# Performance work log

Hardware: AMD Instinct MI355X
Metric: run time of the kernel (lower is better)

Reference implementation:

```python
import jax, jax.numpy as jnp
import numpy as np

CUTOFF = 5.0
NUM_RADIAL = 6
HIDDEN = 128
N_NODES = 100000
N_EDGES = 800000
MAX_Z = 95
P = 6  # envelope_exponent(5) + 1, per PyG Envelope


def _envelope(x):
    # PyG DimeNet Envelope: (1/x + a*x^(p-1) + b*x^p + c*x^(p+1)) * (x < 1)
    a = -(P + 1) * (P + 2) / 2.0   # -28
    b = P * (P + 2)                # 48
    c = -P * (P + 1) / 2.0         # -21
    xp0 = x ** (P - 1)
    xp1 = xp0 * x
    xp2 = xp1 * x
    return (1.0 / x + a * xp0 + b * xp1 + c * xp2) * (x < 1.0)


def setup_inputs():
    key = jax.random.key(0)
    ks = jax.random.split(key, 8)
    z = jax.random.randint(ks[0], (N_NODES,), 0, MAX_Z, dtype=jnp.int32)
    pos = jax.random.normal(ks[1], (N_NODES, 3), dtype=jnp.float32)
    ei = jax.random.randint(ks[2], (2, N_EDGES), 0, N_NODES, dtype=jnp.int32)
    i, j = ei[0], ei[1]
    j = jnp.where(j == i, (j + 1) % N_NODES, j)  # radius_graph emits no self-loops (avoids d=0)
    edge_index = jnp.stack([i, j])
    # BesselBasisLayer learnable frequencies: pi * n
    freq = np.pi * jnp.arange(1, NUM_RADIAL + 1, dtype=jnp.float32)
    s3 = float(np.sqrt(3.0))
    emb_table = jax.random.uniform(ks[3], (MAX_Z, HIDDEN), jnp.float32, -s3, s3)
    W_rbf = jax.random.normal(ks[4], (NUM_RADIAL, HIDDEN), jnp.float32) * (1.0 / np.sqrt(NUM_RADIAL))
    b_rbf = jnp.zeros((HIDDEN,), jnp.float32)
    W_lin = jax.random.normal(ks[5], (3 * HIDDEN, HIDDEN), jnp.float32) * (1.0 / np.sqrt(3 * HIDDEN))
    b_lin = jnp.zeros((HIDDEN,), jnp.float32)
    return {"z": z, "pos": pos, "edge_index": edge_index, "freq": freq,
            "emb_table": emb_table, "W_rbf": W_rbf, "b_rbf": b_rbf,
            "W_lin": W_lin, "b_lin": b_lin}


def reference(z, pos, edge_index, freq, emb_table, W_rbf, b_rbf, W_lin, b_lin):
    n = z.shape[0]
    i, j = edge_index[0], edge_index[1]
    # per-edge distance  [E]
    d = jnp.sqrt(jnp.sum((pos[i] - pos[j]) ** 2, axis=-1))
    # Bessel RBF  [E, num_radial]
    x = d[:, None] / CUTOFF
    rbf = _envelope(x) * jnp.sin(freq * x)
    # DimeNet EmbeddingBlock (act = SiLU/swish)
    h_rbf = jax.nn.silu(rbf @ W_rbf + b_rbf)            # [E, H]
    xz = emb_table[z]                                    # [N, H]
    e_emb = jax.nn.silu(
        jnp.concatenate([xz[i], xz[j], h_rbf], axis=-1) @ W_lin + b_lin
    )                                                    # [E, H]
    # scatter_mean over target node j -> [N, H]
    sums = jax.ops.segment_sum(e_emb, j, num_segments=n)
    cnt = jax.ops.segment_sum(jnp.ones_like(d), j, num_segments=n)
    v_emb = sums / jnp.maximum(cnt, 1.0)[:, None]
    return v_emb  # pool=None -> node-level embeddings
```

## Files before the change

kernel.cpp:

```cpp
#include <hip/hip_runtime.h>
#include <hip/hip_bf16.h>
#include <math.h>

#define HID 128
#define NRAD 6
#define TABN 4096
#define CUTOFF_INV 0.2f
#define MZ 95
#define MZP (MZ + 1)
#define SENT ((MZ << 13) | (MZ << 20))
#define PAD 32
#define OVF_CAP 65536
#define FTR 8
#define LOG2E 1.4426950408889634f
#define LN2   0.6931471805599453f

typedef unsigned int uint32;
typedef __attribute__((ext_vector_type(2))) float f2;

__global__ void build1(const float* __restrict__ emb, const float* __restrict__ W_lin,
                       const float* __restrict__ freq, const float* __restrict__ W_rbf,
                       const float* __restrict__ b_rbf, const float* __restrict__ b_lin,
                       const int* __restrict__ ei, const float* __restrict__ pos,
                       const int* __restrict__ z,
                       __hip_bfloat16* __restrict__ Tb, float* __restrict__ ftab,
                       int* __restrict__ cnt, int* __restrict__ payload,
                       int* __restrict__ ovfcnt, int2* __restrict__ ovfbuf,
                       int MAXZ, int E) {
    __shared__ float sh[FTR * HID];
    int h   = threadIdx.x;
    int bid = blockIdx.x;
    int nT  = 2 * (MAXZ + 1);
    int nF  = (TABN + FTR) / FTR;
    if (bid < nT) {
        int zz = bid >> 1, s = bid & 1;
        if (zz == MAXZ) {
            Tb[(size_t)(s * (MAXZ + 1) + zz) * HID + h] = __float2bfloat16(-86.5f);
            return;
        }
        sh[h] = emb[zz * HID + h];
        __syncthreads();
        const float* W = W_lin + (size_t)s * HID * HID;
        float acc = (s == 0) ? b_lin[h] : 0.f;
#pragma unroll 8
        for (int k = 0; k < HID; ++k) acc = fmaf(sh[k], W[k * HID + h], acc);
        Tb[(size_t)(s * (MAXZ + 1) + zz) * HID + h] = __float2bfloat16(acc * LOG2E);
    } else if (bid < nT + nF) {
        int t0 = (bid - nT) * FTR;
        for (int r = 0; r < FTR; ++r) {
            int t = t0 + r;
            float rbf[NRAD];
            if (t == 0) {
#pragma unroll
                for (int k = 0; k < NRAD; ++k) rbf[k] = freq[k];
            } else if (t >= TABN) {
#pragma unroll
                for (int k = 0; k < NRAD; ++k) rbf[k] = 0.f;
            } else {
                float x  = (float)t / (float)TABN;
                float x2 = x * x, x5 = x2 * x2 * x;
                float env = 1.f / x + x5 * (-28.f + x * (48.f + x * (-21.f)));
#pragma unroll
                for (int k = 0; k < NRAD; ++k) rbf[k] = env * sinf(freq[k] * x);
            }
            float pre = b_rbf[h];
#pragma unroll
            for (int k = 0; k < NRAD; ++k) pre = fmaf(rbf[k], W_rbf[k * HID + h], pre);
            sh[r * HID + h] = pre / (1.f + __expf(-pre));
        }
        __syncthreads();
        const float* W3 = W_lin + (size_t)2 * HID * HID;
        float acc[FTR];
#pragma unroll
        for (int r = 0; r < FTR; ++r) acc[r] = 0.f;
#pragma unroll 4
        for (int k = 0; k < HID; ++k) {
            float w = W3[k * HID + h];
#pragma unroll
            for (int r = 0; r < FTR; ++r) acc[r] = fmaf(sh[r * HID + k], w, acc[r]);
        }
        for (int r = 0; r < FTR; ++r) {
            int t = t0 + r;
            if (t <= TABN) ftab[(size_t)t * HID + h] = acc[r] * LOG2E;
        }
    } else {
        int e = (bid - nT - nF) * HID + h;
        if (e < E) {
            int i = ei[e];
            int j = ei[E + e];
            float dx = pos[3 * i]     - pos[3 * j];
            float dy = pos[3 * i + 1] - pos[3 * j + 1];
            float dz = pos[3 * i + 2] - pos[3 * j + 2];
            float d  = sqrtf(dx * dx + dy * dy + dz * dz);
            float u  = fminf(d * CUTOFF_INV, 1.0f) * (float)TABN;
            int   ti = (int)(u + 0.5f);
            if (ti > TABN) ti = TABN;
            int pl = ti | (z[i] << 13) | (z[j] << 20);
            int r  = atomicAdd(&cnt[j], 1);
            if (r < PAD) {
                payload[(size_t)j * PAD + r] = pl;
            } else {
                int o = atomicAdd(ovfcnt, 1);
                if (o < OVF_CAP) ovfbuf[o] = make_int2(j, pl);
            }
        }
    }
}

__device__ __forceinline__ float exp2neg(float x) {
    float r; asm("v_exp_f32 %0, -%1" : "=v"(r) : "v"(x)); return r;
}

#define RL(pv_, idx_) __builtin_amdgcn_readlane((pv_), (idx_))

#define FLOAD(pl_) (*(const f2*)((const char*)ftab + (uint32)((((pl_) & 0x1FFF) << 9) + fbyte)))

#define TLA(pl_) sT[((((pl_) >> 13) & 0x7F) << 6) + lane]
#define TLB(pl_) sT[sB + ((((pl_) >> 20) & 0x7F) << 6) + lane]

#define COMPUTE(f_, ua_, ub_) do {                                             \
    f2 A_, B_, P_, E_, R_;                                                     \
    A_.x = __uint_as_float((ua_) << 16);                                       \
    A_.y = __uint_as_float((ua_) & 0xFFFF0000u);                               \
    B_.x = __uint_as_float((ub_) << 16);                                       \
    B_.y = __uint_as_float((ub_) & 0xFFFF0000u);                               \
    P_ = (A_ + B_) + f_;                                  \
    E_.x = exp2neg(P_.x);  E_.y = exp2neg(P_.y);                               \
    E_ = E_ + onev;                                              \
    R_.x = __builtin_amdgcn_rcpf(E_.x);                                        \
    R_.y = __builtin_amdgcn_rcpf(E_.y);                                        \
    acc = __builtin_elementwise_fma(P_, R_, acc);            \
} while (0)

__launch_bounds__(1024)
__global__ void gather_k(const int* __restrict__ cnt, const int* __restrict__ payload,
                         const uint32* __restrict__ Tb32, const float* __restrict__ ftab,
                         const int* __restrict__ ovfcnt, const int2* __restrict__ ovfbuf,
                         float* __restrict__ out, int N) {
    __shared__ uint32 sT[2 * MZP * (HID / 2)];
    int tid = threadIdx.x;
    for (int k = tid; k < 2 * MZP * (HID / 2); k += 1024) sT[k] = Tb32[k];
    __syncthreads();

    const int sB = MZP * (HID / 2);
    int lane = tid & 63;
    int l32  = lane & 31;
    int wv   = __builtin_amdgcn_readfirstlane(tid >> 6);
    uint32 fbyte = (uint32)lane << 3;
    f2 onev; onev.x = 1.f; onev.y = 1.f;
    int nov  = __builtin_amdgcn_readfirstlane(*ovfcnt);
    if (nov > OVF_CAP) nov = OVF_CAP;
    int nW = gridDim.x << 4;

    int n = (blockIdx.x << 4) + wv;
    int degC = 0, plvC = SENT;
    if (n < N) {
        degC = __builtin_amdgcn_readfirstlane(cnt[n]);
        plvC = payload[(size_t)n * PAD + l32];
    }

    while (n < N) {
        int n2 = n + nW;
        int degN = 0, plvN = SENT;
        if (n2 < N) {
            degN = __builtin_amdgcn_readfirstlane(cnt[n2]);
            plvN = payload[(size_t)n2 * PAD + l32];
        }

        int deg = degC;
        int cb  = deg < PAD ? deg : PAD;
        int plv = (l32 < cb) ? plvC : SENT;

        f2 acc; acc.x = 0.f; acc.y = 0.f;
        if (cb > 0) {
            int pl0 = RL(plv, 0), pl1 = RL(plv, 1), pl2 = RL(plv, 2);
            f2 g0 = FLOAD(pl0), g1 = FLOAD(pl1), g2 = FLOAD(pl2);
            uint32 ua0 = TLA(pl0), ub0 = TLB(pl0);
            uint32 ua1 = TLA(pl1), ub1 = TLB(pl1);
#pragma unroll 4
            for (int k = 0; k < cb; ++k) {
                int pl3 = RL(plv, k + 3);
                f2 g3 = FLOAD(pl3);
                uint32 ua2 = TLA(pl2), ub2 = TLB(pl2);
                COMPUTE(g0, ua0, ub0);
                g0 = g1; g1 = g2; g2 = g3;
                ua0 = ua1; ub0 = ub1;
                ua1 = ua2; ub1 = ub2;
                pl2 = pl3;
            }
        }
        if (deg > PAD && nov > 0) {
            for (int o = 0; o < nov; ++o) {
                int2 v = ovfbuf[o];
                int jn = __builtin_amdgcn_readfirstlane(v.x);
                if (jn == n) {
                    int pl = __builtin_amdgcn_readfirstlane(v.y);
                    f2 f_ = FLOAD(pl);
                    uint32 ua_ = TLA(pl), ub_ = TLB(pl);
                    COMPUTE(f_, ua_, ub_);
                }
            }
        }
        float s = (deg > 0) ? LN2 / (float)deg : 0.0f;
        f2 o2; o2.x = acc.x * s; o2.y = acc.y * s;
        *(f2*)(out + (size_t)n * HID + (lane << 1)) = o2;
        n = n2; degC = degN; plvC = plvN;
    }
}

extern "C" void kernel_launch(void* const* d_in, const int* in_sizes, int n_in,
                              void* d_out, int out_size, void* d_ws, size_t ws_size,
                              hipStream_t stream) {
    const int*   z     = (const int*)d_in[0];
    const float* pos   = (const float*)d_in[1];
    const int*   ei    = (const int*)d_in[2];
    const float* freq  = (const float*)d_in[3];
    const float* emb   = (const float*)d_in[4];
    const float* W_rbf = (const float*)d_in[5];
    const float* b_rbf = (const float*)d_in[6];
    const float* W_lin = (const float*)d_in[7];
    const float* b_lin = (const float*)d_in[8];

    int N    = in_sizes[0];
    int E    = in_sizes[2] / 2;
    int MAXZ = in_sizes[4] / HID;
    float* out = (float*)d_out;

    int N_pad = ((N + 1024) / 1024) * 1024;

    char* ws = (char*)d_ws;
    size_t off = 0;
    auto alloc = [&](size_t bytes) { char* p = ws + off; off = (off + bytes + 255) & ~(size_t)255; return p; };
    int*   cnt     = (int*)alloc((size_t)N_pad * 4);
    int*   ovfcnt  = (int*)alloc(256);
    __hip_bfloat16* Tb = (__hip_bfloat16*)alloc((size_t)2 * (MAXZ + 1) * HID * 2);
    float* ftab    = (float*)alloc((size_t)(TABN + 1) * HID * 4);
    int*   payload = (int*)alloc((size_t)N_pad * PAD * 4);
    int2*  ovfbuf  = (int2*)alloc((size_t)OVF_CAP * 8);

    hipMemsetAsync(cnt, 0, (size_t)N_pad * 4 + 256, stream);

    int nBuild = 2 * (MAXZ + 1) + (TABN + FTR) / FTR + (E + HID - 1) / HID;
    build1<<<nBuild, HID, 0, stream>>>(emb, W_lin, freq, W_rbf, b_rbf, b_lin,
                                       ei, pos, z, Tb, ftab, cnt, payload,
                                       ovfcnt, ovfbuf, MAXZ, E);
    gather_k<<<512, 1024, 0, stream>>>(cnt, payload, (const uint32*)Tb, ftab,
                                       ovfcnt, ovfbuf, out, N);
}
```

Baseline: 178.6 us.

## Pack pos and z into float4, hoist target-node table term out of gather loop

```diff
diff --git a/kernel.cpp b/kernel.cpp
--- a/kernel.cpp
+++ b/kernel.cpp
@@ -8,7 +8,7 @@
 #define CUTOFF_INV 0.2f
 #define MZ 95
 #define MZP (MZ + 1)
-#define SENT ((MZ << 13) | (MZ << 20))
+#define SENTI (MZ << 13)
 #define PAD 32
 #define OVF_CAP 65536
 #define FTR 8
@@ -18,11 +18,26 @@
 typedef unsigned int uint32;
 typedef __attribute__((ext_vector_type(2))) float f2;
 
+__global__ void zpack_k(const float* __restrict__ pos, const int* __restrict__ z,
+                        float4* __restrict__ pos4, int* __restrict__ cnt,
+                        int* __restrict__ ovfcnt, int N) {
+    int n = blockIdx.x * 256 + threadIdx.x;
+    if (blockIdx.x == 0 && threadIdx.x == 0) *ovfcnt = 0;
+    if (n < N) {
+        float4 p;
+        p.x = pos[3 * n];
+        p.y = pos[3 * n + 1];
+        p.z = pos[3 * n + 2];
+        p.w = __int_as_float(z[n]);
+        pos4[n] = p;
+        cnt[n]  = 0;
+    }
+}
+
 __global__ void build1(const float* __restrict__ emb, const float* __restrict__ W_lin,
                        const float* __restrict__ freq, const float* __restrict__ W_rbf,
                        const float* __restrict__ b_rbf, const float* __restrict__ b_lin,
-                       const int* __restrict__ ei, const float* __restrict__ pos,
-                       const int* __restrict__ z,
+                       const int* __restrict__ ei, const float4* __restrict__ pos4,
                        __hip_bfloat16* __restrict__ Tb, float* __restrict__ ftab,
                        int* __restrict__ cnt, int* __restrict__ payload,
                        int* __restrict__ ovfcnt, int2* __restrict__ ovfbuf,
@@ -84,24 +99,36 @@
             if (t <= TABN) ftab[(size_t)t * HID + h] = acc[r] * LOG2E;
         }
     } else {
-        int e = (bid - nT - nF) * HID + h;
-        if (e < E) {
-            int i = ei[e];
-            int j = ei[E + e];
-            float dx = pos[3 * i]     - pos[3 * j];
-            float dy = pos[3 * i + 1] - pos[3 * j + 1];
-            float dz = pos[3 * i + 2] - pos[3 * j + 2];
-            float d  = sqrtf(dx * dx + dy * dy + dz * dz);
-            float u  = fminf(d * CUTOFF_INV, 1.0f) * (float)TABN;
-            int   ti = (int)(u + 0.5f);
-            if (ti > TABN) ti = TABN;
-            int pl = ti | (z[i] << 13) | (z[j] << 20);
-            int r  = atomicAdd(&cnt[j], 1);
-            if (r < PAD) {
-                payload[(size_t)j * PAD + r] = pl;
-            } else {
-                int o = atomicAdd(ovfcnt, 1);
-                if (o < OVF_CAP) ovfbuf[o] = make_int2(j, pl);
+        int t  = (bid - nT - nF) * HID + h;
+        int Eh = (E + 1) >> 1;
+        if (t < Eh) {
+            int  e1   = t + Eh;
+            bool has1 = e1 < E;
+            int i0 = ei[t],  j0 = ei[E + t];
+            int i1 = has1 ? ei[e1] : i0, j1 = has1 ? ei[E + e1] : j0;
+            float4 a0 = pos4[i0], b0 = pos4[j0];
+            float4 a1 = pos4[i1], b1 = pos4[j1];
+
+            float dx0 = a0.x - b0.x, dy0 = a0.y - b0.y, dz0 = a0.z - b0.z;
+            float d0  = sqrtf(dx0 * dx0 + dy0 * dy0 + dz0 * dz0);
+            float u0  = fminf(d0 * CUTOFF_INV, 1.0f) * (float)TABN;
+            int   ti0 = (int)(u0 + 0.5f);
+            if (ti0 > TABN) ti0 = TABN;
+            int pl0 = ti0 | (__float_as_int(a0.w) << 13);
+            int r0  = atomicAdd(&cnt[j0], 1);
+            if (r0 < PAD) payload[(size_t)j0 * PAD + r0] = pl0;
+            else { int o = atomicAdd(ovfcnt, 1); if (o < OVF_CAP) ovfbuf[o] = make_int2(j0, pl0); }
+
+            if (has1) {
+                float dx1 = a1.x - b1.x, dy1 = a1.y - b1.y, dz1 = a1.z - b1.z;
+                float d1  = sqrtf(dx1 * dx1 + dy1 * dy1 + dz1 * dz1);
+                float u1  = fminf(d1 * CUTOFF_INV, 1.0f) * (float)TABN;
+                int   ti1 = (int)(u1 + 0.5f);
+                if (ti1 > TABN) ti1 = TABN;
+                int pl1 = ti1 | (__float_as_int(a1.w) << 13);
+                int r1  = atomicAdd(&cnt[j1], 1);
+                if (r1 < PAD) payload[(size_t)j1 * PAD + r1] = pl1;
+                else { int o = atomicAdd(ovfcnt, 1); if (o < OVF_CAP) ovfbuf[o] = make_int2(j1, pl1); }
             }
         }
     }
@@ -116,15 +143,12 @@
 #define FLOAD(pl_) (*(const f2*)((const char*)ftab + (uint32)((((pl_) & 0x1FFF) << 9) + fbyte)))
 
 #define TLA(pl_) sT[((((pl_) >> 13) & 0x7F) << 6) + lane]
-#define TLB(pl_) sT[sB + ((((pl_) >> 20) & 0x7F) << 6) + lane]
-
-#define COMPUTE(f_, ua_, ub_) do {                                             \
-    f2 A_, B_, P_, E_, R_;                                                     \
+
+#define COMPUTE(f_, ua_) do {                                                  \
+    f2 A_, P_, E_, R_;                                                         \
     A_.x = __uint_as_float((ua_) << 16);                                       \
     A_.y = __uint_as_float((ua_) & 0xFFFF0000u);                               \
-    B_.x = __uint_as_float((ub_) << 16);                                       \
-    B_.y = __uint_as_float((ub_) & 0xFFFF0000u);                               \
-    P_ = (A_ + B_) + f_;                                  \
+    P_ = (A_ + Bv) + f_;                                  \
     E_.x = exp2neg(P_.x);  E_.y = exp2neg(P_.y);                               \
     E_ = E_ + onev;                                              \
     R_.x = __builtin_amdgcn_rcpf(E_.x);                                        \
@@ -135,14 +159,15 @@
 __launch_bounds__(1024)
 __global__ void gather_k(const int* __restrict__ cnt, const int* __restrict__ payload,
                          const uint32* __restrict__ Tb32, const float* __restrict__ ftab,
+                         const int* __restrict__ z,
                          const int* __restrict__ ovfcnt, const int2* __restrict__ ovfbuf,
                          float* __restrict__ out, int N) {
-    __shared__ uint32 sT[2 * MZP * (HID / 2)];
+    __shared__ uint32 sT[MZP * (HID / 2)];
     int tid = threadIdx.x;
-    for (int k = tid; k < 2 * MZP * (HID / 2); k += 1024) sT[k] = Tb32[k];
+    for (int k = tid; k < MZP * (HID / 2); k += 1024) sT[k] = Tb32[k];
     __syncthreads();
 
-    const int sB = MZP * (HID / 2);
+    const uint32* T2g = Tb32 + MZP * (HID / 2);
     int lane = tid & 63;
     int l32  = lane & 31;
     int wv   = __builtin_amdgcn_readfirstlane(tid >> 6);
@@ -153,39 +178,45 @@
     int nW = gridDim.x << 4;
 
     int n = (blockIdx.x << 4) + wv;
-    int degC = 0, plvC = SENT;
+    int degC = 0, plvC = SENTI; uint32 ubC = 0;
     if (n < N) {
         degC = __builtin_amdgcn_readfirstlane(cnt[n]);
         plvC = payload[(size_t)n * PAD + l32];
+        int zn = __builtin_amdgcn_readfirstlane(z[n]);
+        ubC  = T2g[(zn << 6) + lane];
     }
 
     while (n < N) {
         int n2 = n + nW;
-        int degN = 0, plvN = SENT;
+        int degN = 0, plvN = SENTI; uint32 ubN = 0;
         if (n2 < N) {
             degN = __builtin_amdgcn_readfirstlane(cnt[n2]);
             plvN = payload[(size_t)n2 * PAD + l32];
+            int zn2 = __builtin_amdgcn_readfirstlane(z[n2]);
+            ubN  = T2g[(zn2 << 6) + lane];
         }
 
         int deg = degC;
         int cb  = deg < PAD ? deg : PAD;
-        int plv = (l32 < cb) ? plvC : SENT;
+        int plv = (l32 < cb) ? plvC : SENTI;
+        f2 Bv;
+        Bv.x = __uint_as_float(ubC << 16);
+        Bv.y = __uint_as_float(ubC & 0xFFFF0000u);
 
         f2 acc; acc.x = 0.f; acc.y = 0.f;
         if (cb > 0) {
             int pl0 = RL(plv, 0), pl1 = RL(plv, 1), pl2 = RL(plv, 2);
             f2 g0 = FLOAD(pl0), g1 = FLOAD(pl1), g2 = FLOAD(pl2);
-            uint32 ua0 = TLA(pl0), ub0 = TLB(pl0);
-            uint32 ua1 = TLA(pl1), ub1 = TLB(pl1);
+            uint32 ua0 = TLA(pl0);
+            uint32 ua1 = TLA(pl1);
 #pragma unroll 4
             for (int k = 0; k < cb; ++k) {
                 int pl3 = RL(plv, k + 3);
                 f2 g3 = FLOAD(pl3);
-                uint32 ua2 = TLA(pl2), ub2 = TLB(pl2);
-                COMPUTE(g0, ua0, ub0);
+                uint32 ua2 = TLA(pl2);
+                COMPUTE(g0, ua0);
                 g0 = g1; g1 = g2; g2 = g3;
-                ua0 = ua1; ub0 = ub1;
-                ua1 = ua2; ub1 = ub2;
+                ua0 = ua1; ua1 = ua2;
                 pl2 = pl3;
             }
         }
@@ -196,15 +227,15 @@
                 if (jn == n) {
                     int pl = __builtin_amdgcn_readfirstlane(v.y);
                     f2 f_ = FLOAD(pl);
-                    uint32 ua_ = TLA(pl), ub_ = TLB(pl);
-                    COMPUTE(f_, ua_, ub_);
+                    uint32 ua_ = TLA(pl);
+                    COMPUTE(f_, ua_);
                 }
             }
         }
         float s = (deg > 0) ? LN2 / (float)deg : 0.0f;
         f2 o2; o2.x = acc.x * s; o2.y = acc.y * s;
         *(f2*)(out + (size_t)n * HID + (lane << 1)) = o2;
-        n = n2; degC = degN; plvC = plvN;
+        n = n2; degC = degN; plvC = plvN; ubC = ubN;
     }
 }
 
@@ -237,13 +268,15 @@
     float* ftab    = (float*)alloc((size_t)(TABN + 1) * HID * 4);
     int*   payload = (int*)alloc((size_t)N_pad * PAD * 4);
     int2*  ovfbuf  = (int2*)alloc((size_t)OVF_CAP * 8);
-
-    hipMemsetAsync(cnt, 0, (size_t)N_pad * 4 + 256, stream);
-
-    int nBuild = 2 * (MAXZ + 1) + (TABN + FTR) / FTR + (E + HID - 1) / HID;
+    float4* pos4   = (float4*)alloc((size_t)N_pad * 16);
+
+    zpack_k<<<(N + 255) / 256, 256, 0, stream>>>(pos, z, pos4, cnt, ovfcnt, N);
+
+    int Eh = (E + 1) / 2;
+    int nBuild = 2 * (MAXZ + 1) + (TABN + FTR) / FTR + (Eh + HID - 1) / HID;
     build1<<<nBuild, HID, 0, stream>>>(emb, W_lin, freq, W_rbf, b_rbf, b_lin,
-                                       ei, pos, z, Tb, ftab, cnt, payload,
+                                       ei, pos4, Tb, ftab, cnt, payload,
                                        ovfcnt, ovfbuf, MAXZ, E);
-    gather_k<<<512, 1024, 0, stream>>>(cnt, payload, (const uint32*)Tb, ftab,
+    gather_k<<<512, 1024, 0, stream>>>(cnt, payload, (const uint32*)Tb, ftab, z,
                                        ovfcnt, ovfbuf, out, N);
 }
```

Result: no change. 180.3 us (+1.0%).
